# Kernel tuning notes

Measured on AMD Instinct MI355X. Metric: run time of the kernel, lower is better.

## Reference

```python
import jax, jax.numpy as jnp
import numpy as np


def setup_inputs() -> dict:
    key = jax.random.key(0)
    k1, k2, k3, k4 = jax.random.split(key, 4)
    B, S, K, N = 4, 2048, 4096, 4096
    # int8-valued quantized activations / weights (held in int32 containers)
    a = jax.random.randint(k1, (B, S, K), -128, 128, dtype=jnp.int32)
    w = jax.random.randint(k2, (K, N), -128, 128, dtype=jnp.int32)
    # per-token activation scale and per-output-column weight scale
    a_scale = jax.random.uniform(k3, (B, S, 1), dtype=jnp.float32) * 0.01
    w_scale = jax.random.uniform(k4, (1, N), dtype=jnp.float32) * 0.01
    return {"a": a, "a_scale": a_scale, "w": w, "w_scale": w_scale}


def reference(a, a_scale, w, w_scale):
    # int8 GEMM with int32 accumulation (torch._int_mm equivalent),
    # batched over B instead of a per-slice Python loop.
    acc = jnp.einsum("bsk,kn->bsn", a, w)  # int32 accumulate
    # dequant epilogue: out = acc * (a_scale * w_scale), then cast to model dtype
    out = acc.astype(jnp.float32) * (a_scale * w_scale)  # [B,S,N]
    return out.astype(jnp.float32)
```

## Files before the change

### kernel.cpp

```cpp
#include <hip/hip_runtime.h>


#define M_TOT 8192
#define N_TOT 4096
#define K_TOT 4096
#define NT_K  (K_TOT / 64)
#define TILE_BYTES 16384

typedef int v4i  __attribute__((ext_vector_type(4)));
typedef int v16i __attribute__((ext_vector_type(16)));

typedef const __attribute__((address_space(1))) unsigned char* gas1_t;
typedef __attribute__((address_space(3))) unsigned char* las3_t;

__global__ __launch_bounds__(256) void pack_a_kernel(const int* __restrict__ a,
                                                     unsigned char* __restrict__ a8) {
    const int tile = blockIdx.x;
    const int kt = tile & (NT_K - 1);
    const int mt = tile >> 6;
    const int t = threadIdx.x;
    unsigned char* outp = a8 + (size_t)tile * TILE_BYTES;
    const int* rowp = a + (size_t)(mt * 256 + t) * K_TOT + kt * 64;
#pragma unroll
    for (int slot = 0; slot < 4; ++slot) {
        const int* src = rowp + slot * 16;
        int4 v0 = ((const int4*)src)[0];
        int4 v1 = ((const int4*)src)[1];
        int4 v2 = ((const int4*)src)[2];
        int4 v3 = ((const int4*)src)[3];
        int4 p;
        p.x = (int)((unsigned)(v0.x & 255) | ((unsigned)(v0.y & 255) << 8) |
                    ((unsigned)(v0.z & 255) << 16) | ((unsigned)v0.w << 24));
        p.y = (int)((unsigned)(v1.x & 255) | ((unsigned)(v1.y & 255) << 8) |
                    ((unsigned)(v1.z & 255) << 16) | ((unsigned)v1.w << 24));
        p.z = (int)((unsigned)(v2.x & 255) | ((unsigned)(v2.y & 255) << 8) |
                    ((unsigned)(v2.z & 255) << 16) | ((unsigned)v2.w << 24));
        p.w = (int)((unsigned)(v3.x & 255) | ((unsigned)(v3.y & 255) << 8) |
                    ((unsigned)(v3.z & 255) << 16) | ((unsigned)v3.w << 24));
        *(int4*)(outp + slot * 4096 + t * 16) = p;
    }
}

__global__ __launch_bounds__(256) void pack_w_kernel(const int* __restrict__ w,
                                                     unsigned char* __restrict__ w8) {
    const int tile = blockIdx.x;
    const int kt = tile & (NT_K - 1);
    const int nt = tile >> 6;
    const int t = threadIdx.x;
    unsigned char* outp = w8 + (size_t)tile * TILE_BYTES;
#pragma unroll
    for (int slot = 0; slot < 4; ++slot) {
        const int* src = w + (size_t)(kt * 64 + slot * 16) * N_TOT + nt * 256 + t;
        int b[16];
#pragma unroll
        for (int j = 0; j < 16; ++j) b[j] = src[(size_t)j * N_TOT];
        int4 p;
        p.x = (int)((unsigned)(b[0] & 255) | ((unsigned)(b[1] & 255) << 8) |
                    ((unsigned)(b[2] & 255) << 16) | ((unsigned)b[3] << 24));
        p.y = (int)((unsigned)(b[4] & 255) | ((unsigned)(b[5] & 255) << 8) |
                    ((unsigned)(b[6] & 255) << 16) | ((unsigned)b[7] << 24));
        p.z = (int)((unsigned)(b[8] & 255) | ((unsigned)(b[9] & 255) << 8) |
                    ((unsigned)(b[10] & 255) << 16) | ((unsigned)b[11] << 24));
        p.w = (int)((unsigned)(b[12] & 255) | ((unsigned)(b[13] & 255) << 8) |
                    ((unsigned)(b[14] & 255) << 16) | ((unsigned)b[15] << 24));
        *(int4*)(outp + slot * 4096 + t * 16) = p;
    }
}

__global__ __launch_bounds__(512, 2) void gemm_i8_kernel(
    const unsigned char* __restrict__ a8, const unsigned char* __restrict__ w8,
    const float* __restrict__ a_scale, const float* __restrict__ w_scale,
    float* __restrict__ out) {

    __shared__ __attribute__((aligned(16))) unsigned char sm[2][2][TILE_BYTES];

    const int t = threadIdx.x;
    const int lane = t & 63;
    const int wid = t >> 6;
    const int wr = wid >> 2;
    const int wc = wid & 3;
    const int hi = lane >> 5;
    const int lo32 = lane & 31;

    int bid = blockIdx.x;
    bid = (bid & 7) * (512 / 8) + (bid >> 3);
    const int mt = bid >> 4;
    const int nt = bid & 15;

    const unsigned char* a_tiles = a8 + (size_t)mt * NT_K * TILE_BYTES;
    const unsigned char* w_tiles = w8 + (size_t)nt * NT_K * TILE_BYTES;

    v16i acc[4][2] = {};

#define STAGE_CHUNK(pbuf, op, half, gsrc)                                         \
    __builtin_amdgcn_global_load_lds((gas1_t)((gsrc) + (half) * 8192 + t * 16),   \
        (las3_t)&sm[pbuf][op][(half) * 8192 + t * 16], 16, 0, 0)

#define PHASE(buf, kc, gaN, gbN) do {                                             \
    const unsigned char* lA = &sm[buf][0][0];                                     \
    const unsigned char* lB = &sm[buf][1][0];                                     \
    const int so = ((kc) * 2 + hi) * 4096;                                        \
    v4i af[4], bf[2];                                                             \
    _Pragma("unroll")                                                             \
    for (int mi = 0; mi < 4; ++mi)                                                \
        af[mi] = *(const v4i*)(lA + so + (wr * 128 + mi * 32 + lo32) * 16);       \
    _Pragma("unroll")                                                             \
    for (int ni = 0; ni < 2; ++ni)                                                \
        bf[ni] = *(const v4i*)(lB + so + (wc * 64 + ni * 32 + lo32) * 16);        \
    STAGE_CHUNK((buf) ^ 1, 0, (kc), gaN);                                         \
    STAGE_CHUNK((buf) ^ 1, 1, (kc), gbN);                                         \
    asm volatile("s_waitcnt vmcnt(2)" ::: "memory");                              \
    __builtin_amdgcn_s_barrier();                                                 \
    asm volatile("s_waitcnt lgkmcnt(0)" ::: "memory");                            \
    __builtin_amdgcn_sched_barrier(0);                                            \
    __builtin_amdgcn_s_setprio(1);                                                \
    _Pragma("unroll")                                                             \
    for (int mi = 0; mi < 4; ++mi)                                                \
        _Pragma("unroll")                                                         \
        for (int ni = 0; ni < 2; ++ni)                                            \
            acc[mi][ni] = __builtin_amdgcn_mfma_i32_32x32x32_i8(                  \
                af[mi], bf[ni], acc[mi][ni], 0, 0, 0);                            \
    __builtin_amdgcn_s_setprio(0);                                                \
    __builtin_amdgcn_s_barrier();                                                 \
} while (0)

    STAGE_CHUNK(0, 0, 0, a_tiles);
    STAGE_CHUNK(0, 1, 0, w_tiles);
    STAGE_CHUNK(0, 0, 1, a_tiles);
    STAGE_CHUNK(0, 1, 1, w_tiles);
    asm volatile("s_waitcnt vmcnt(2)" ::: "memory");
    __builtin_amdgcn_s_barrier();

#pragma unroll 1
    for (int T = 0; T < NT_K; T += 2) {
        const int Tn1 = (T + 1 < NT_K) ? T + 1 : NT_K - 1;
        const int Tn2 = (T + 2 < NT_K) ? T + 2 : NT_K - 1;
        const unsigned char* ga1 = a_tiles + (size_t)Tn1 * TILE_BYTES;
        const unsigned char* gb1 = w_tiles + (size_t)Tn1 * TILE_BYTES;
        const unsigned char* ga2 = a_tiles + (size_t)Tn2 * TILE_BYTES;
        const unsigned char* gb2 = w_tiles + (size_t)Tn2 * TILE_BYTES;
        PHASE(0, 0, ga1, gb1);
        PHASE(0, 1, ga1, gb1);
        PHASE(1, 0, ga2, gb2);
        PHASE(1, 1, ga2, gb2);
    }

    asm volatile("s_waitcnt vmcnt(0)" ::: "memory");

#undef STAGE_CHUNK
#undef PHASE

    const int row0 = mt * 256 + wr * 128;
    const int col0 = nt * 256 + wc * 64;
#pragma unroll
    for (int mi = 0; mi < 4; ++mi) {
#pragma unroll
        for (int r = 0; r < 16; ++r) {
            const int row = row0 + mi * 32 + (r & 3) + 8 * (r >> 2) + 4 * hi;
            const float as = a_scale[row];
            float* orow = out + (size_t)row * N_TOT + col0 + lo32;
#pragma unroll
            for (int ni = 0; ni < 2; ++ni)
                orow[ni * 32] = (float)acc[mi][ni][r] * as * w_scale[col0 + ni * 32 + lo32];
        }
    }
}

extern "C" void kernel_launch(void* const* d_in, const int* in_sizes, int n_in,
                              void* d_out, int out_size, void* d_ws, size_t ws_size,
                              hipStream_t stream) {
    const int*   a       = (const int*)d_in[0];
    const float* a_scale = (const float*)d_in[1];
    const int*   w       = (const int*)d_in[2];
    const float* w_scale = (const float*)d_in[3];
    float*       out     = (float*)d_out;

    unsigned char* a8 = (unsigned char*)d_ws;
    unsigned char* w8 = a8 + (size_t)M_TOT * K_TOT;

    pack_a_kernel<<<(M_TOT / 256) * NT_K, 256, 0, stream>>>(a, a8);
    pack_w_kernel<<<(N_TOT / 256) * NT_K, 256, 0, stream>>>(w, w8);
    gemm_i8_kernel<<<(M_TOT / 256) * (N_TOT / 256), 512, 0, stream>>>(
        a8, w8, a_scale, w_scale, out);
}
```

Measured before the change: 422.6 us.

## Coalesce pack kernels via LDS staging and triple-buffer GEMM K-tiles

The pack kernels now load contiguous int4 rows into shared memory, using an XOR swizzle for A, and then pack bytes from LDS. This replaces the previous per-thread strided global reads, which coalesced poorly, especially the column-strided reads of W. The GEMM moves from double-buffered half-tile staging to a three-deep ring of full K-tiles with prefetch distance two, so each barrier pair covers 16 MFMAs instead of 8. LDS use rises to 96KB per block, which may limit occupancy to fewer than the 2 blocks per CU the launch bounds request.

```diff
diff --git a/kernel.cpp b/kernel.cpp
--- a/kernel.cpp
+++ b/kernel.cpp
@@ -13,57 +13,69 @@
 typedef const __attribute__((address_space(1))) unsigned char* gas1_t;
 typedef __attribute__((address_space(3))) unsigned char* las3_t;
 
+__device__ __forceinline__ int pack4(int4 v) {
+    return (int)((unsigned)(v.x & 255) | ((unsigned)(v.y & 255) << 8) |
+                 ((unsigned)(v.z & 255) << 16) | ((unsigned)v.w << 24));
+}
+
 __global__ __launch_bounds__(256) void pack_a_kernel(const int* __restrict__ a,
                                                      unsigned char* __restrict__ a8) {
+    __shared__ int4 stage[256 * 16];
     const int tile = blockIdx.x;
     const int kt = tile & (NT_K - 1);
     const int mt = tile >> 6;
     const int t = threadIdx.x;
+#pragma unroll
+    for (int i = 0; i < 16; ++i) {
+        const int idx16 = i * 256 + t;
+        const int r = idx16 >> 4;
+        const int c = idx16 & 15;
+        int4 v = *(const int4*)(a + (size_t)(mt * 256 + r) * K_TOT + kt * 64 + c * 4);
+        stage[r * 16 + (c ^ (r & 15))] = v;
+    }
+    __syncthreads();
     unsigned char* outp = a8 + (size_t)tile * TILE_BYTES;
-    const int* rowp = a + (size_t)(mt * 256 + t) * K_TOT + kt * 64;
-#pragma unroll
-    for (int slot = 0; slot < 4; ++slot) {
-        const int* src = rowp + slot * 16;
-        int4 v0 = ((const int4*)src)[0];
-        int4 v1 = ((const int4*)src)[1];
-        int4 v2 = ((const int4*)src)[2];
-        int4 v3 = ((const int4*)src)[3];
-        int4 p;
-        p.x = (int)((unsigned)(v0.x & 255) | ((unsigned)(v0.y & 255) << 8) |
-                    ((unsigned)(v0.z & 255) << 16) | ((unsigned)v0.w << 24));
-        p.y = (int)((unsigned)(v1.x & 255) | ((unsigned)(v1.y & 255) << 8) |
-                    ((unsigned)(v1.z & 255) << 16) | ((unsigned)v1.w << 24));
-        p.z = (int)((unsigned)(v2.x & 255) | ((unsigned)(v2.y & 255) << 8) |
-                    ((unsigned)(v2.z & 255) << 16) | ((unsigned)v2.w << 24));
-        p.w = (int)((unsigned)(v3.x & 255) | ((unsigned)(v3.y & 255) << 8) |
-                    ((unsigned)(v3.z & 255) << 16) | ((unsigned)v3.w << 24));
-        *(int4*)(outp + slot * 4096 + t * 16) = p;
+#pragma unroll
+    for (int j = 0; j < 4; ++j) {
+        int4 d0 = stage[t * 16 + ((j * 4 + 0) ^ (t & 15))];
+        int4 d1 = stage[t * 16 + ((j * 4 + 1) ^ (t & 15))];
+        int4 d2 = stage[t * 16 + ((j * 4 + 2) ^ (t & 15))];
+        int4 d3 = stage[t * 16 + ((j * 4 + 3) ^ (t & 15))];
+        int4 p = { pack4(d0), pack4(d1), pack4(d2), pack4(d3) };
+        *(int4*)(outp + j * 4096 + t * 16) = p;
     }
 }
 
 __global__ __launch_bounds__(256) void pack_w_kernel(const int* __restrict__ w,
                                                      unsigned char* __restrict__ w8) {
+    __shared__ int stage[64 * 256];
     const int tile = blockIdx.x;
     const int kt = tile & (NT_K - 1);
     const int nt = tile >> 6;
     const int t = threadIdx.x;
+#pragma unroll
+    for (int i = 0; i < 16; ++i) {
+        const int idx = i * 256 + t;
+        const int k = idx >> 6;
+        const int c4 = idx & 63;
+        int4 v = *(const int4*)(w + (size_t)(kt * 64 + k) * N_TOT + nt * 256 + c4 * 4);
+        *(int4*)&stage[k * 256 + c4 * 4] = v;
+    }
+    __syncthreads();
     unsigned char* outp = w8 + (size_t)tile * TILE_BYTES;
 #pragma unroll
-    for (int slot = 0; slot < 4; ++slot) {
-        const int* src = w + (size_t)(kt * 64 + slot * 16) * N_TOT + nt * 256 + t;
-        int b[16];
-#pragma unroll
-        for (int j = 0; j < 16; ++j) b[j] = src[(size_t)j * N_TOT];
+    for (int j = 0; j < 4; ++j) {
         int4 p;
-        p.x = (int)((unsigned)(b[0] & 255) | ((unsigned)(b[1] & 255) << 8) |
-                    ((unsigned)(b[2] & 255) << 16) | ((unsigned)b[3] << 24));
-        p.y = (int)((unsigned)(b[4] & 255) | ((unsigned)(b[5] & 255) << 8) |
-                    ((unsigned)(b[6] & 255) << 16) | ((unsigned)b[7] << 24));
-        p.z = (int)((unsigned)(b[8] & 255) | ((unsigned)(b[9] & 255) << 8) |
-                    ((unsigned)(b[10] & 255) << 16) | ((unsigned)b[11] << 24));
-        p.w = (int)((unsigned)(b[12] & 255) | ((unsigned)(b[13] & 255) << 8) |
-                    ((unsigned)(b[14] & 255) << 16) | ((unsigned)b[15] << 24));
-        *(int4*)(outp + slot * 4096 + t * 16) = p;
+#pragma unroll
+        for (int qq = 0; qq < 4; ++qq) {
+            int4 b;
+            b.x = stage[(j * 16 + qq * 4 + 0) * 256 + t];
+            b.y = stage[(j * 16 + qq * 4 + 1) * 256 + t];
+            b.z = stage[(j * 16 + qq * 4 + 2) * 256 + t];
+            b.w = stage[(j * 16 + qq * 4 + 3) * 256 + t];
+            ((int*)&p)[qq] = pack4(b);
+        }
+        *(int4*)(outp + j * 4096 + t * 16) = p;
     }
 }
 
@@ -72,7 +84,7 @@
     const float* __restrict__ a_scale, const float* __restrict__ w_scale,
     float* __restrict__ out) {
 
-    __shared__ __attribute__((aligned(16))) unsigned char sm[2][2][TILE_BYTES];
+    __shared__ __attribute__((aligned(16))) unsigned char sm[3][2][TILE_BYTES];
 
     const int t = threadIdx.x;
     const int lane = t & 63;
@@ -92,63 +104,70 @@
 
     v16i acc[4][2] = {};
 
-#define STAGE_CHUNK(pbuf, op, half, gsrc)                                         \
-    __builtin_amdgcn_global_load_lds((gas1_t)((gsrc) + (half) * 8192 + t * 16),   \
-        (las3_t)&sm[pbuf][op][(half) * 8192 + t * 16], 16, 0, 0)
-
-#define PHASE(buf, kc, gaN, gbN) do {                                             \
-    const unsigned char* lA = &sm[buf][0][0];                                     \
-    const unsigned char* lB = &sm[buf][1][0];                                     \
-    const int so = ((kc) * 2 + hi) * 4096;                                        \
-    v4i af[4], bf[2];                                                             \
+#define STAGE_TILE(b2, gaP, gbP) do {                                             \
+    __builtin_amdgcn_global_load_lds((gas1_t)((gaP) + t * 16),                    \
+        (las3_t)&sm[b2][0][t * 16], 16, 0, 0);                                    \
+    __builtin_amdgcn_global_load_lds((gas1_t)((gaP) + 8192 + t * 16),             \
+        (las3_t)&sm[b2][0][8192 + t * 16], 16, 0, 0);                             \
+    __builtin_amdgcn_global_load_lds((gas1_t)((gbP) + t * 16),                    \
+        (las3_t)&sm[b2][1][t * 16], 16, 0, 0);                                    \
+    __builtin_amdgcn_global_load_lds((gas1_t)((gbP) + 8192 + t * 16),             \
+        (las3_t)&sm[b2][1][8192 + t * 16], 16, 0, 0);                             \
+} while (0)
+
+#define ITER(b0, b2, Tcur) do {                                                   \
+    const int Tp = ((Tcur) + 2 <= NT_K - 1) ? (Tcur) + 2 : NT_K - 1;              \
+    STAGE_TILE(b2, a_tiles + (size_t)Tp * TILE_BYTES,                             \
+                   w_tiles + (size_t)Tp * TILE_BYTES);                            \
+    v4i af[2][4], bf[2][2];                                                       \
+    const unsigned char* lA = &sm[b0][0][0];                                      \
+    const unsigned char* lB = &sm[b0][1][0];                                      \
     _Pragma("unroll")                                                             \
-    for (int mi = 0; mi < 4; ++mi)                                                \
-        af[mi] = *(const v4i*)(lA + so + (wr * 128 + mi * 32 + lo32) * 16);       \
-    _Pragma("unroll")                                                             \
-    for (int ni = 0; ni < 2; ++ni)                                                \
-        bf[ni] = *(const v4i*)(lB + so + (wc * 64 + ni * 32 + lo32) * 16);        \
-    STAGE_CHUNK((buf) ^ 1, 0, (kc), gaN);                                         \
-    STAGE_CHUNK((buf) ^ 1, 1, (kc), gbN);                                         \
-    asm volatile("s_waitcnt vmcnt(2)" ::: "memory");                              \
+    for (int kc = 0; kc < 2; ++kc) {                                              \
+        const int so = (kc * 2 + hi) * 4096;                                      \
+        _Pragma("unroll")                                                         \
+        for (int mi = 0; mi < 4; ++mi)                                            \
+            af[kc][mi] = *(const v4i*)(lA + so + (wr * 128 + mi * 32 + lo32) * 16);\
+        _Pragma("unroll")                                                         \
+        for (int ni = 0; ni < 2; ++ni)                                            \
+            bf[kc][ni] = *(const v4i*)(lB + so + (wc * 64 + ni * 32 + lo32) * 16);\
+    }                                                                             \
+    asm volatile("s_waitcnt vmcnt(4)" ::: "memory");                              \
     __builtin_amdgcn_s_barrier();                                                 \
     asm volatile("s_waitcnt lgkmcnt(0)" ::: "memory");                            \
     __builtin_amdgcn_sched_barrier(0);                                            \
     __builtin_amdgcn_s_setprio(1);                                                \
     _Pragma("unroll")                                                             \
-    for (int mi = 0; mi < 4; ++mi)                                                \
+    for (int kc = 0; kc < 2; ++kc)                                                \
         _Pragma("unroll")                                                         \
-        for (int ni = 0; ni < 2; ++ni)                                            \
-            acc[mi][ni] = __builtin_amdgcn_mfma_i32_32x32x32_i8(                  \
-                af[mi], bf[ni], acc[mi][ni], 0, 0, 0);                            \
+        for (int mi = 0; mi < 4; ++mi)                                            \
+            _Pragma("unroll")                                                     \
+            for (int ni = 0; ni < 2; ++ni)                                        \
+                acc[mi][ni] = __builtin_amdgcn_mfma_i32_32x32x32_i8(              \
+                    af[kc][mi], bf[kc][ni], acc[mi][ni], 0, 0, 0);                \
     __builtin_amdgcn_s_setprio(0);                                                \
     __builtin_amdgcn_s_barrier();                                                 \
 } while (0)
 
-    STAGE_CHUNK(0, 0, 0, a_tiles);
-    STAGE_CHUNK(0, 1, 0, w_tiles);
-    STAGE_CHUNK(0, 0, 1, a_tiles);
-    STAGE_CHUNK(0, 1, 1, w_tiles);
-    asm volatile("s_waitcnt vmcnt(2)" ::: "memory");
+    STAGE_TILE(0, a_tiles, w_tiles);
+    STAGE_TILE(1, a_tiles + TILE_BYTES, w_tiles + TILE_BYTES);
+    asm volatile("s_waitcnt vmcnt(4)" ::: "memory");
     __builtin_amdgcn_s_barrier();
 
+    int T = 0;
 #pragma unroll 1
-    for (int T = 0; T < NT_K; T += 2) {
-        const int Tn1 = (T + 1 < NT_K) ? T + 1 : NT_K - 1;
-        const int Tn2 = (T + 2 < NT_K) ? T + 2 : NT_K - 1;
-        const unsigned char* ga1 = a_tiles + (size_t)Tn1 * TILE_BYTES;
-        const unsigned char* gb1 = w_tiles + (size_t)Tn1 * TILE_BYTES;
-        const unsigned char* ga2 = a_tiles + (size_t)Tn2 * TILE_BYTES;
-        const unsigned char* gb2 = w_tiles + (size_t)Tn2 * TILE_BYTES;
-        PHASE(0, 0, ga1, gb1);
-        PHASE(0, 1, ga1, gb1);
-        PHASE(1, 0, ga2, gb2);
-        PHASE(1, 1, ga2, gb2);
-    }
+    for (int u = 0; u < 21; ++u) {
+        ITER(0, 2, T);
+        ITER(1, 0, T + 1);
+        ITER(2, 1, T + 2);
+        T += 3;
+    }
+    ITER(0, 2, 63);
 
     asm volatile("s_waitcnt vmcnt(0)" ::: "memory");
 
-#undef STAGE_CHUNK
-#undef PHASE
+#undef STAGE_TILE
+#undef ITER
 
     const int row0 = mt * 256 + wr * 128;
     const int col0 = nt * 256 + wc * 64;
```

After: 402.3 us. 4.8% less time.
